# Kernel tuning notes

Measured on AMD Instinct MI355X. Metric: run time of the kernel, lower is better.

The kernel has to match this reference:

```python
import jax, jax.numpy as jnp
import numpy as np

D_CH = 2048  # channels
N = 64       # hidden_state
L = 8192     # sequence length
MIN_DELTA, MAX_DELTA = 1e-3, 0.1


def setup_inputs() -> dict:
    key = jax.random.key(0)
    ks = jax.random.split(key, 5)
    X = jax.random.normal(ks[0], (D_CH, L), jnp.float32)
    # kaiming_normal_(nonlinearity='linear'): std = 1/sqrt(fan_in=N)
    A = jax.random.normal(ks[1], (N, N), jnp.float32) * (1.0 / N) ** 0.5
    B = jax.random.normal(ks[2], (N, D_CH), jnp.float32) * (1.0 / N) ** 0.5
    C = jax.random.normal(ks[3], (D_CH, N), jnp.float32)
    Dp = jnp.ones((D_CH,), jnp.float32)
    log_delta = jax.random.uniform(ks[4], (1,), jnp.float32,
                                   float(np.log(MIN_DELTA)), float(np.log(MAX_DELTA)))
    return {"X": X, "A": A, "B": B, "C": C, "Dp": Dp, "log_delta": log_delta}


def reference(X, A, B, C, Dp, log_delta):
    # X: (D, L). Bilinear (Tustin) discretization with dt = exp(log_delta).
    n = A.shape[0]
    delta = jnp.exp(log_delta)[0]
    I = jnp.eye(n, dtype=A.dtype)
    inv = jnp.linalg.inv(I - (delta * 0.5) * A)
    dA = inv @ (I + (delta * 0.5) * A)      # (N, N)
    dB = delta * (inv @ B)                   # (N, D)

    def step(h, x_t):
        # h: (N,), x_t: (D,)
        h = dA @ h + dB @ x_t
        return h, C @ h                      # y_t: (D,)

    h0 = jnp.zeros((n,), X.dtype)
    _, ys = jax.lax.scan(step, h0, X.T)      # ys: (L, D)
    # skip connection y += D * X (per-channel)
    return ys.T + Dp[:, None] * X            # (D, L)
```

## Files before the change

kernel.cpp:

```cpp
#include <hip/hip_runtime.h>
#include <math.h>

#define D_CH 2048
#define LSEQ 8192
#define T1 32
#define NC1 256
#define VSLAB 524288

typedef __attribute__((ext_vector_type(8))) short bf16x8;
typedef __attribute__((ext_vector_type(4))) float f32x4;

__device__ __forceinline__ short f2bf(float x) {
  unsigned u = __float_as_uint(x);
  u += 0x7FFFu + ((u >> 16) & 1);
  return (short)(u >> 16);
}

__device__ __forceinline__ void mmzero(float acc[16]) {
#pragma unroll
  for (int t = 0; t < 16; ++t) acc[t] = 0.f;
}

template <int SZ>
__device__ __forceinline__ void mmld(float acc[16], const float* __restrict__ Z,
                                     int r0, int c0) {
#pragma unroll
  for (int i = 0; i < 4; ++i) {
    float4 z = *(const float4*)&Z[(r0 + i) * SZ + c0];
    acc[i * 4 + 0] = z.x; acc[i * 4 + 1] = z.y;
    acc[i * 4 + 2] = z.z; acc[i * 4 + 3] = z.w;
  }
}

template <int SX, int SY>
__device__ __forceinline__ void mac44(float acc[16], const float* __restrict__ Xb,
                                      const float* __restrict__ Yb, int r0, int c0) {
#pragma unroll 4
  for (int k = 0; k < 64; k += 4) {
    float4 x0 = *(const float4*)&Xb[(r0 + 0) * SX + k];
    float4 x1 = *(const float4*)&Xb[(r0 + 1) * SX + k];
    float4 x2 = *(const float4*)&Xb[(r0 + 2) * SX + k];
    float4 x3 = *(const float4*)&Xb[(r0 + 3) * SX + k];
    float4 y0 = *(const float4*)&Yb[(k + 0) * SY + c0];
    float4 y1 = *(const float4*)&Yb[(k + 1) * SY + c0];
    float4 y2 = *(const float4*)&Yb[(k + 2) * SY + c0];
    float4 y3 = *(const float4*)&Yb[(k + 3) * SY + c0];
#define MROW(i, xi) \
    acc[i * 4 + 0] += xi.x * y0.x + xi.y * y1.x + xi.z * y2.x + xi.w * y3.x; \
    acc[i * 4 + 1] += xi.x * y0.y + xi.y * y1.y + xi.z * y2.y + xi.w * y3.y; \
    acc[i * 4 + 2] += xi.x * y0.z + xi.y * y1.z + xi.z * y2.z + xi.w * y3.z; \
    acc[i * 4 + 3] += xi.x * y0.w + xi.y * y1.w + xi.z * y2.w + xi.w * y3.w;
    MROW(0, x0) MROW(1, x1) MROW(2, x2) MROW(3, x3)
#undef MROW
  }
}

template <int SZ>
__device__ __forceinline__ void mmst(float* Dst, const float acc[16], int r0, int c0) {
#pragma unroll
  for (int i = 0; i < 4; ++i)
    *(float4*)&Dst[(r0 + i) * SZ + c0] =
        make_float4(acc[i * 4 + 0], acc[i * 4 + 1], acc[i * 4 + 2], acc[i * 4 + 3]);
}

__global__ __launch_bounds__(256) void main_kernel(const float* __restrict__ X,
                                                   const float* __restrict__ A,
                                                   const float* __restrict__ B,
                                                   const float* __restrict__ logd,
                                                   float* __restrict__ invdT,
                                                   float* __restrict__ dAg,
                                                   float* __restrict__ V,
                                                   int KS) {
  __shared__ float smem[8704];
  const int tid = threadIdx.x;
  const int lane = tid & 63;
  const int w = tid >> 6;

  if (blockIdx.x == 0) {
    float* bQ = smem;
    float* bP = smem + 4352;
    const int r0 = (tid >> 4) * 4, c0 = (tid & 15) * 4;
    const float delta = expf(logd[0]);
    const float half = 0.5f * delta;
    float accQ[16], accP[16];

    for (int idx = tid; idx < 4096; idx += 256) {
      int i = idx >> 6, j = idx & 63;
      float p = half * A[idx];
      bP[i * 68 + j] = p;
      bQ[i * 68 + j] = p + (i == j ? 1.f : 0.f);
    }
    __syncthreads();
    mmzero(accP); mac44<68, 68>(accP, bP, bP, r0, c0);
    __syncthreads();
    mmst<68>(bP, accP, r0, c0);
    __syncthreads();
#pragma unroll 1
    for (int s = 0; s < 3; ++s) {
      mmld<68>(accQ, bQ, r0, c0);
      mac44<68, 68>(accQ, bP, bQ, r0, c0);
      if (s < 2) { mmzero(accP); mac44<68, 68>(accP, bP, bP, r0, c0); }
      __syncthreads();
      mmst<68>(bQ, accQ, r0, c0);
      if (s < 2) mmst<68>(bP, accP, r0, c0);
      __syncthreads();
    }

    for (int idx = tid; idx < 4096; idx += 256) {
      int n = idx >> 6, m = idx & 63;
      float qv = bQ[n * 68 + m];
      invdT[m * 64 + n] = delta * qv;
      dAg[idx] = 2.f * qv - (n == m ? 1.f : 0.f);
    }
    return;
  }

  const int b = blockIdx.x - 1;
  const int t0 = (b & 255) << 5;
  const int slab = b >> 8;
  const int k0 = slab * KS;
  short* Xs = (short*)smem;
  short* Bs = (short*)smem + 2304;
  const int q = lane >> 4, r = lane & 15;
  const int hi = lane >> 5, tl = lane & 31;
  const int brow = lane >> 3;
  const int bkc = (lane & 7) * 8;
  const int wm = (w & 1) * 16;
  const int wn = (w >> 1) * 32;

  f32x4 acc[2];
#pragma unroll
  for (int j = 0; j < 2; ++j) acc[j] = (f32x4){0.f, 0.f, 0.f, 0.f};

  float xv[8];
  float bv[16];

#define LOADX(KK)                                                              \
  _Pragma("unroll")                                                            \
  for (int j = 0; j < 8; ++j)                                                  \
    xv[j] = X[(size_t)(k0 + (KK) + w * 16 + hi * 8 + j) * LSEQ + t0 + tl];

#define LOADB(KK)                                                              \
  _Pragma("unroll")                                                            \
  for (int p = 0; p < 2; ++p) {                                                \
    int n = p * 32 + w * 8 + brow;                                             \
    float4 f0 = *(const float4*)&B[(size_t)n * D_CH + k0 + (KK) + bkc];        \
    float4 f1 = *(const float4*)&B[(size_t)n * D_CH + k0 + (KK) + bkc + 4];    \
    bv[p * 8 + 0] = f0.x; bv[p * 8 + 1] = f0.y;                                \
    bv[p * 8 + 2] = f0.z; bv[p * 8 + 3] = f0.w;                                \
    bv[p * 8 + 4] = f1.x; bv[p * 8 + 5] = f1.y;                                \
    bv[p * 8 + 6] = f1.z; bv[p * 8 + 7] = f1.w;                                \
  }

  LOADX(0)
  LOADB(0)

  for (int kk = 0; kk < KS; kk += 64) {
    bf16x8 xp;
#pragma unroll
    for (int j = 0; j < 8; ++j) xp[j] = f2bf(xv[j]);
    *(bf16x8*)&Xs[tl * 72 + w * 16 + hi * 8] = xp;
#pragma unroll
    for (int p = 0; p < 2; ++p) {
      bf16x8 bp8;
#pragma unroll
      for (int j = 0; j < 8; ++j) bp8[j] = f2bf(bv[p * 8 + j]);
      *(bf16x8*)&Bs[(p * 32 + w * 8 + brow) * 72 + bkc] = bp8;
    }
    __syncthreads();

    if (kk + 64 < KS) {
      LOADX(kk + 64)
      LOADB(kk + 64)
    }

#pragma unroll
    for (int ks = 0; ks < 64; ks += 32) {
      bf16x8 a = *(const bf16x8*)&Xs[(wm + r) * 72 + ks + q * 8];
#pragma unroll
      for (int j = 0; j < 2; ++j) {
        bf16x8 bb = *(const bf16x8*)&Bs[(wn + j * 16 + r) * 72 + ks + q * 8];
        acc[j] = __builtin_amdgcn_mfma_f32_16x16x32_bf16(a, bb, acc[j], 0, 0, 0);
      }
    }
    __syncthreads();
  }
#undef LOADX
#undef LOADB

  float* Vs = V + (size_t)slab * VSLAB;
#pragma unroll
  for (int j = 0; j < 2; ++j)
#pragma unroll
    for (int reg = 0; reg < 4; ++reg)
      Vs[(size_t)(t0 + wm + q * 4 + reg) * 64 + wn + j * 16 + r] = acc[j][reg];
}

__device__ __forceinline__ float matvec_lds(const float* __restrict__ Mrow,
                                            const float* __restrict__ hb, float u) {
  float a0 = u, a1 = 0.f, a2 = 0.f, a3 = 0.f;
#pragma unroll
  for (int jj = 0; jj < 64; jj += 4) {
    float4 m = *(const float4*)&Mrow[jj];
    float4 hv = *(const float4*)&hb[jj];
    a0 += m.x * hv.x;
    a1 += m.y * hv.y;
    a2 += m.z * hv.z;
    a3 += m.w * hv.w;
  }
  return (a0 + a1) + (a2 + a3);
}

__device__ __forceinline__ void stage_mat64(float* Mlds, const float* __restrict__ Mg,
                                            int lane) {
#pragma unroll
  for (int i = 0; i < 16; ++i) {
    int row = i * 4 + (lane >> 4);
    int col = (lane & 15) * 4;
    *(float4*)&Mlds[row * 68 + col] = *(const float4*)&Mg[row * 64 + col];
  }
  __syncthreads();
}

__global__ __launch_bounds__(256) void scan1_kernel(const float* __restrict__ V,
                                                    const float* __restrict__ invdT,
                                                    const float* __restrict__ dA,
                                                    float* __restrict__ U,
                                                    float* __restrict__ S,
                                                    float* __restrict__ dA32g,
                                                    float* __restrict__ dA512g,
                                                    int nslab) {
  __shared__ float smem[13056];
  const int tid = threadIdx.x;
  const int c = blockIdx.x;

  if (c == NC1) {
    float* b0 = smem;
    float* b1 = smem + 4352;
    const int r0 = (tid >> 4) * 4, c0 = (tid & 15) * 4;
    for (int idx = tid; idx < 4096; idx += 256)
      b0[(idx >> 6) * 68 + (idx & 63)] = dA[idx];
    __syncthreads();
    float acc[16];
    float* p = b0; float* q = b1;
    for (int s = 1; s <= 9; ++s) {
      mmzero(acc); mac44<68, 68>(acc, p, p, r0, c0);
      if (s == 5) mmst<64>(dA32g, acc, r0, c0);
      if (s == 9) mmst<64>(dA512g, acc, r0, c0);
      mmst<68>(q, acc, r0, c0);
      __syncthreads();
      float* t = p; p = q; q = t;
    }
    return;
  }

  float* invs = smem;
  float* Vs   = smem + 4096;
  float* Us   = smem + 6144;
  float* hs0  = smem + 8192;
  float* hs1  = smem + 8256;
  float* Md   = smem + 8320;

  for (int idx = tid; idx < 4096; idx += 256) invs[idx] = invdT[idx];
  for (int idx = tid; idx < 4096; idx += 256)
    Md[(idx >> 6) * 68 + (idx & 63)] = dA[idx];
  for (int idx = tid; idx < 2048; idx += 256) {
    float v = 0.f;
    for (int s = 0; s < nslab; ++s) v += V[(size_t)s * VSLAB + (size_t)c * 2048 + idx];
    Vs[idx] = v;
  }
  __syncthreads();

  const int r0 = (tid >> 4) * 2, c0 = (tid & 15) * 4;
  float a0[4] = {0.f, 0.f, 0.f, 0.f}, a1[4] = {0.f, 0.f, 0.f, 0.f};
#pragma unroll 4
  for (int k = 0; k < 64; k += 4) {
    float4 v0 = *(const float4*)&Vs[r0 * 64 + k];
    float4 v1 = *(const float4*)&Vs[(r0 + 1) * 64 + k];
    float4 y0 = *(const float4*)&invs[(k + 0) * 64 + c0];
    float4 y1 = *(const float4*)&invs[(k + 1) * 64 + c0];
    float4 y2 = *(const float4*)&invs[(k + 2) * 64 + c0];
    float4 y3 = *(const float4*)&invs[(k + 3) * 64 + c0];
    a0[0] += v0.x * y0.x + v0.y * y1.x + v0.z * y2.x + v0.w * y3.x;
    a0[1] += v0.x * y0.y + v0.y * y1.y + v0.z * y2.y + v0.w * y3.y;
    a0[2] += v0.x * y0.z + v0.y * y1.z + v0.z * y2.z + v0.w * y3.z;
    a0[3] += v0.x * y0.w + v0.y * y1.w + v0.z * y2.w + v0.w * y3.w;
    a1[0] += v1.x * y0.x + v1.y * y1.x + v1.z * y2.x + v1.w * y3.x;
    a1[1] += v1.x * y0.y + v1.y * y1.y + v1.z * y2.y + v1.w * y3.y;
    a1[2] += v1.x * y0.z + v1.y * y1.z + v1.z * y2.z + v1.w * y3.z;
    a1[3] += v1.x * y0.w + v1.y * y1.w + v1.z * y2.w + v1.w * y3.w;
  }
  *(float4*)&Us[r0 * 64 + c0] = make_float4(a0[0], a0[1], a0[2], a0[3]);
  *(float4*)&Us[(r0 + 1) * 64 + c0] = make_float4(a1[0], a1[1], a1[2], a1[3]);
  *(float4*)&U[(size_t)(c * 32 + r0) * 64 + c0] = make_float4(a0[0], a0[1], a0[2], a0[3]);
  *(float4*)&U[(size_t)(c * 32 + r0 + 1) * 64 + c0] = make_float4(a1[0], a1[1], a1[2], a1[3]);
  __syncthreads();

  if (tid < 64) {
    const float* row = Md + tid * 68;
    float h = 0.f;
    hs0[tid] = 0.f;
    for (int t = 0; t < T1; ++t) {
      float u = Us[t * 64 + tid];
      h = matvec_lds(row, (t & 1) ? hs1 : hs0, u);
      ((t & 1) ? hs0 : hs1)[tid] = h;
    }
    S[c * 64 + tid] = h;
  }
}

__global__ __launch_bounds__(64) void mid1_kernel(const float* __restrict__ S,
                                                  const float* __restrict__ dA32,
                                                  float* __restrict__ S2g) {
  __shared__ float M[64 * 68];
  __shared__ float hs[2][64];
  const int lane = threadIdx.x;
  const int g = blockIdx.x;
  stage_mat64(M, dA32, lane);
  const float* row = M + lane * 68;
  const float* in = S + g * 16 * 64;
  float h = 0.f;
  hs[0][lane] = 0.f;
  for (int t = 0; t < 16; ++t) {
    h = matvec_lds(row, hs[t & 1], in[t * 64 + lane]);
    hs[(t + 1) & 1][lane] = h;
  }
  S2g[g * 64 + lane] = h;
}

__global__ __launch_bounds__(64) void mid2_kernel(const float* __restrict__ S2g,
                                                  const float* __restrict__ dA512,
                                                  float* __restrict__ H2g) {
  __shared__ float M[64 * 68];
  __shared__ float hs[2][64];
  const int lane = threadIdx.x;
  stage_mat64(M, dA512, lane);
  const float* row = M + lane * 68;
  float h = 0.f;
  hs[0][lane] = 0.f;
  for (int t = 0; t < 16; ++t) {
    H2g[t * 64 + lane] = h;
    h = matvec_lds(row, hs[t & 1], S2g[t * 64 + lane]);
    hs[(t + 1) & 1][lane] = h;
  }
}

__global__ __launch_bounds__(64) void mid3_kernel(const float* __restrict__ S,
                                                  const float* __restrict__ dA32,
                                                  const float* __restrict__ H2g,
                                                  float* __restrict__ Hinit) {
  __shared__ float M[64 * 68];
  __shared__ float hs[2][64];
  const int lane = threadIdx.x;
  const int g = blockIdx.x;
  stage_mat64(M, dA32, lane);
  const float* row = M + lane * 68;
  const float* in = S + g * 16 * 64;
  float h = H2g[g * 64 + lane];
  hs[0][lane] = h;
  for (int t = 0; t < 16; ++t) {
    Hinit[(g * 16 + t) * 64 + lane] = h;
    h = matvec_lds(row, hs[t & 1], in[t * 64 + lane]);
    hs[(t + 1) & 1][lane] = h;
  }
}

__global__ __launch_bounds__(64) void scan2_kernel(const float* __restrict__ U,
                                                   const float* __restrict__ dA,
                                                   const float* __restrict__ Hinit,
                                                   float* __restrict__ Ht) {
  __shared__ float M[64 * 68];
  __shared__ float hs[2][64];
  const int tid = threadIdx.x;
  const int c = blockIdx.x;
  stage_mat64(M, dA, tid);
  const float* row = M + tid * 68;
  float h = Hinit[c * 64 + tid];
  hs[0][tid] = h;
  const float* inc = U + (size_t)c * T1 * 64;
  float* outc = Ht + (size_t)c * T1 * 64;
  float up[4];
#pragma unroll
  for (int i = 0; i < 4; ++i) up[i] = inc[i * 64 + tid];

  for (int t = 0; t < T1; ++t) {
    float u = up[t & 3];
    if (t + 4 < T1) up[t & 3] = inc[(t + 4) * 64 + tid];
    h = matvec_lds(row, hs[t & 1], u);
    hs[(t + 1) & 1][tid] = h;
    outc[t * 64 + tid] = h;
  }
}

__global__ __launch_bounds__(256) void out_kernel(const float* __restrict__ X,
                                                  const float* __restrict__ C,
                                                  const float* __restrict__ Dp,
                                                  const float* __restrict__ Ht,
                                                  float* __restrict__ Y) {
  __shared__ short Cs[64 * 72];
  __shared__ short Hs[64 * 72];
  const int tid = threadIdx.x;
  const int lane = tid & 63, w = tid >> 6;
  const int t0 = blockIdx.x * 64;
  const int d0 = blockIdx.y * 64;
  const int q = lane >> 4, r = lane & 15;
  const int brow = lane >> 3, bkc = (lane & 7) * 8;

#pragma unroll
  for (int p = 0; p < 2; ++p) {
    int row = p * 32 + w * 8 + brow;
    float4 c0 = *(const float4*)&C[(size_t)(d0 + row) * 64 + bkc];
    float4 c1 = *(const float4*)&C[(size_t)(d0 + row) * 64 + bkc + 4];
    float4 h0 = *(const float4*)&Ht[(size_t)(t0 + row) * 64 + bkc];
    float4 h1 = *(const float4*)&Ht[(size_t)(t0 + row) * 64 + bkc + 4];
    bf16x8 cv, hv;
    cv[0] = f2bf(c0.x); cv[1] = f2bf(c0.y); cv[2] = f2bf(c0.z); cv[3] = f2bf(c0.w);
    cv[4] = f2bf(c1.x); cv[5] = f2bf(c1.y); cv[6] = f2bf(c1.z); cv[7] = f2bf(c1.w);
    hv[0] = f2bf(h0.x); hv[1] = f2bf(h0.y); hv[2] = f2bf(h0.z); hv[3] = f2bf(h0.w);
    hv[4] = f2bf(h1.x); hv[5] = f2bf(h1.y); hv[6] = f2bf(h1.z); hv[7] = f2bf(h1.w);
    *(bf16x8*)&Cs[row * 72 + bkc] = cv;
    *(bf16x8*)&Hs[row * 72 + bkc] = hv;
  }
  __syncthreads();

  f32x4 acc[4];
#pragma unroll
  for (int j = 0; j < 4; ++j) acc[j] = (f32x4){0.f, 0.f, 0.f, 0.f};
#pragma unroll
  for (int ks = 0; ks < 64; ks += 32) {
    bf16x8 a = *(const bf16x8*)&Cs[(w * 16 + r) * 72 + ks + q * 8];
#pragma unroll
    for (int j = 0; j < 4; ++j) {
      bf16x8 bb = *(const bf16x8*)&Hs[(j * 16 + r) * 72 + ks + q * 8];
      acc[j] = __builtin_amdgcn_mfma_f32_16x16x32_bf16(a, bb, acc[j], 0, 0, 0);
    }
  }

#pragma unroll
  for (int reg = 0; reg < 4; ++reg) {
    int d = d0 + w * 16 + q * 4 + reg;
    float dp = Dp[d];
#pragma unroll
    for (int j = 0; j < 4; ++j) {
      int t = t0 + j * 16 + r;
      size_t off = (size_t)d * LSEQ + t;
      Y[off] = acc[j][reg] + dp * X[off];
    }
  }
}

extern "C" void kernel_launch(void* const* d_in, const int* in_sizes, int n_in,
                              void* d_out, int out_size, void* d_ws, size_t ws_size,
                              hipStream_t stream) {
  const float* X  = (const float*)d_in[0];
  const float* A  = (const float*)d_in[1];
  const float* B  = (const float*)d_in[2];
  const float* Cm = (const float*)d_in[3];
  const float* Dp = (const float*)d_in[4];
  const float* ld = (const float*)d_in[5];
  float* out = (float*)d_out;
  float* ws = (float*)d_ws;

  const size_t need4 =
      (size_t)(16384 + 4 * VSLAB + VSLAB + 16384 + 16384 + 2048) * 4;
  const int nslab = (ws_size >= need4) ? 4 : 2;

  float* invdT = ws;
  float* dA    = ws + 4096;
  float* dA32  = ws + 8192;
  float* dA512 = ws + 12288;
  float* V     = ws + 16384;
  float* U     = V + (size_t)nslab * VSLAB;
  float* S     = U + VSLAB;
  float* Hinit = S + 16384;
  float* S2g   = Hinit + 16384;
  float* H2g   = S2g + 1024;
  float* Ht    = V;

  main_kernel<<<nslab * 256 + 1, 256, 0, stream>>>(X, A, B, ld, invdT, dA, V,
                                                   2048 / nslab);
  scan1_kernel<<<NC1 + 1, 256, 0, stream>>>(V, invdT, dA, U, S, dA32, dA512, nslab);
  mid1_kernel<<<16, 64, 0, stream>>>(S, dA32, S2g);
  mid2_kernel<<<1, 64, 0, stream>>>(S2g, dA512, H2g);
  mid3_kernel<<<16, 64, 0, stream>>>(S, dA32, H2g, Hinit);
  scan2_kernel<<<NC1, 64, 0, stream>>>(U, dA, Hinit, Ht);
  out_kernel<<<dim3(128, 32), 256, 0, stream>>>(X, Cm, Dp, Ht, out);
}
```

Measured before the change: 223.1 us.

## Double-buffer LDS tiles in B*X GEMM and vectorize output epilogue via LDS

The input-projection GEMM now double-buffers its LDS tiles, so the next tile is converted and stored while MFMAs run on the current one. This removes one barrier per k-step. The LDS row pitch changes from 72 to 76 shorts in both GEMM kernels to alter the bank-conflict pattern. The output kernel now stages its accumulators through LDS and writes Y with coalesced float4 loads and stores, replacing the previous scalar strided accesses. These changes cost more LDS and extra barriers in the epilogue.

```diff
diff --git a/kernel.cpp b/kernel.cpp
--- a/kernel.cpp
+++ b/kernel.cpp
@@ -119,8 +119,7 @@
   const int t0 = (b & 255) << 5;
   const int slab = b >> 8;
   const int k0 = slab * KS;
-  short* Xs = (short*)smem;
-  short* Bs = (short*)smem + 2304;
+  short* XB = (short*)smem;
   const int q = lane >> 4, r = lane & 15;
   const int hi = lane >> 5, tl = lane & 31;
   const int brow = lane >> 3;
@@ -142,51 +141,62 @@
 
 #define LOADB(KK)                                                              \
   _Pragma("unroll")                                                            \
-  for (int p = 0; p < 2; ++p) {                                                \
-    int n = p * 32 + w * 8 + brow;                                             \
+  for (int pp = 0; pp < 2; ++pp) {                                             \
+    int n = pp * 32 + w * 8 + brow;                                            \
     float4 f0 = *(const float4*)&B[(size_t)n * D_CH + k0 + (KK) + bkc];        \
     float4 f1 = *(const float4*)&B[(size_t)n * D_CH + k0 + (KK) + bkc + 4];    \
-    bv[p * 8 + 0] = f0.x; bv[p * 8 + 1] = f0.y;                                \
-    bv[p * 8 + 2] = f0.z; bv[p * 8 + 3] = f0.w;                                \
-    bv[p * 8 + 4] = f1.x; bv[p * 8 + 5] = f1.y;                                \
-    bv[p * 8 + 6] = f1.z; bv[p * 8 + 7] = f1.w;                                \
+    bv[pp * 8 + 0] = f0.x; bv[pp * 8 + 1] = f0.y;                              \
+    bv[pp * 8 + 2] = f0.z; bv[pp * 8 + 3] = f0.w;                              \
+    bv[pp * 8 + 4] = f1.x; bv[pp * 8 + 5] = f1.y;                              \
+    bv[pp * 8 + 6] = f1.z; bv[pp * 8 + 7] = f1.w;                              \
+  }
+
+#define STORE_TILE(BUF)                                                        \
+  {                                                                            \
+    short* Xs_ = XB + (BUF) * 7296;                                            \
+    short* Bs_ = Xs_ + 2432;                                                   \
+    bf16x8 xp;                                                                 \
+    _Pragma("unroll")                                                          \
+    for (int j = 0; j < 8; ++j) xp[j] = f2bf(xv[j]);                           \
+    *(bf16x8*)&Xs_[tl * 76 + w * 16 + hi * 8] = xp;                            \
+    _Pragma("unroll")                                                          \
+    for (int pp = 0; pp < 2; ++pp) {                                           \
+      bf16x8 bp8;                                                              \
+      _Pragma("unroll")                                                        \
+      for (int j = 0; j < 8; ++j) bp8[j] = f2bf(bv[pp * 8 + j]);               \
+      *(bf16x8*)&Bs_[(pp * 32 + w * 8 + brow) * 76 + bkc] = bp8;               \
+    }                                                                          \
   }
 
   LOADX(0)
   LOADB(0)
+  STORE_TILE(0)
+  __syncthreads();
 
   for (int kk = 0; kk < KS; kk += 64) {
-    bf16x8 xp;
-#pragma unroll
-    for (int j = 0; j < 8; ++j) xp[j] = f2bf(xv[j]);
-    *(bf16x8*)&Xs[tl * 72 + w * 16 + hi * 8] = xp;
-#pragma unroll
-    for (int p = 0; p < 2; ++p) {
-      bf16x8 bp8;
-#pragma unroll
-      for (int j = 0; j < 8; ++j) bp8[j] = f2bf(bv[p * 8 + j]);
-      *(bf16x8*)&Bs[(p * 32 + w * 8 + brow) * 72 + bkc] = bp8;
-    }
-    __syncthreads();
-
-    if (kk + 64 < KS) {
+    const int cur = (kk >> 6) & 1;
+    const short* Xs = XB + cur * 7296;
+    const short* Bs = Xs + 2432;
+    const bool more = kk + 64 < KS;
+    if (more) {
       LOADX(kk + 64)
       LOADB(kk + 64)
     }
-
 #pragma unroll
     for (int ks = 0; ks < 64; ks += 32) {
-      bf16x8 a = *(const bf16x8*)&Xs[(wm + r) * 72 + ks + q * 8];
+      bf16x8 a = *(const bf16x8*)&Xs[(wm + r) * 76 + ks + q * 8];
 #pragma unroll
       for (int j = 0; j < 2; ++j) {
-        bf16x8 bb = *(const bf16x8*)&Bs[(wn + j * 16 + r) * 72 + ks + q * 8];
+        bf16x8 bb = *(const bf16x8*)&Bs[(wn + j * 16 + r) * 76 + ks + q * 8];
         acc[j] = __builtin_amdgcn_mfma_f32_16x16x32_bf16(a, bb, acc[j], 0, 0, 0);
       }
     }
+    if (more) STORE_TILE(cur ^ 1)
     __syncthreads();
   }
 #undef LOADX
 #undef LOADB
+#undef STORE_TILE
 
   float* Vs = V + (size_t)slab * VSLAB;
 #pragma unroll
@@ -397,8 +407,9 @@
                                                   const float* __restrict__ Dp,
                                                   const float* __restrict__ Ht,
                                                   float* __restrict__ Y) {
-  __shared__ short Cs[64 * 72];
-  __shared__ short Hs[64 * 72];
+  __shared__ float smem[4864];
+  short* Cs = (short*)smem;
+  short* Hs = (short*)smem + 4864;
   const int tid = threadIdx.x;
   const int lane = tid & 63, w = tid >> 6;
   const int t0 = blockIdx.x * 64;
@@ -418,8 +429,8 @@
     cv[4] = f2bf(c1.x); cv[5] = f2bf(c1.y); cv[6] = f2bf(c1.z); cv[7] = f2bf(c1.w);
     hv[0] = f2bf(h0.x); hv[1] = f2bf(h0.y); hv[2] = f2bf(h0.z); hv[3] = f2bf(h0.w);
     hv[4] = f2bf(h1.x); hv[5] = f2bf(h1.y); hv[6] = f2bf(h1.z); hv[7] = f2bf(h1.w);
-    *(bf16x8*)&Cs[row * 72 + bkc] = cv;
-    *(bf16x8*)&Hs[row * 72 + bkc] = hv;
+    *(bf16x8*)&Cs[row * 76 + bkc] = cv;
+    *(bf16x8*)&Hs[row * 76 + bkc] = hv;
   }
   __syncthreads();
 
@@ -428,24 +439,34 @@
   for (int j = 0; j < 4; ++j) acc[j] = (f32x4){0.f, 0.f, 0.f, 0.f};
 #pragma unroll
   for (int ks = 0; ks < 64; ks += 32) {
-    bf16x8 a = *(const bf16x8*)&Cs[(w * 16 + r) * 72 + ks + q * 8];
+    bf16x8 a = *(const bf16x8*)&Cs[(w * 16 + r) * 76 + ks + q * 8];
 #pragma unroll
     for (int j = 0; j < 4; ++j) {
-      bf16x8 bb = *(const bf16x8*)&Hs[(j * 16 + r) * 72 + ks + q * 8];
+      bf16x8 bb = *(const bf16x8*)&Hs[(j * 16 + r) * 76 + ks + q * 8];
       acc[j] = __builtin_amdgcn_mfma_f32_16x16x32_bf16(a, bb, acc[j], 0, 0, 0);
     }
   }
-
-#pragma unroll
-  for (int reg = 0; reg < 4; ++reg) {
-    int d = d0 + w * 16 + q * 4 + reg;
-    float dp = Dp[d];
-#pragma unroll
-    for (int j = 0; j < 4; ++j) {
-      int t = t0 + j * 16 + r;
-      size_t off = (size_t)d * LSEQ + t;
-      Y[off] = acc[j][reg] + dp * X[off];
-    }
+  __syncthreads();
+
+  float* Ts = smem;
+#pragma unroll
+  for (int reg = 0; reg < 4; ++reg)
+#pragma unroll
+    for (int j = 0; j < 4; ++j)
+      Ts[(w * 16 + q * 4 + reg) * 68 + j * 16 + r] = acc[j][reg];
+  __syncthreads();
+
+  const int rr = lane >> 4;
+  const int c4 = (lane & 15) * 4;
+#pragma unroll
+  for (int pass = 0; pass < 4; ++pass) {
+    int row = pass * 16 + w * 4 + rr;
+    float dp = Dp[d0 + row];
+    float4 v = *(const float4*)&Ts[row * 68 + c4];
+    size_t off = (size_t)(d0 + row) * LSEQ + t0 + c4;
+    float4 x = *(const float4*)&X[off];
+    *(float4*)&Y[off] = make_float4(v.x + dp * x.x, v.y + dp * x.y,
+                                    v.z + dp * x.z, v.w + dp * x.w);
   }
 }
 
```

Result: slower. 240.7 us (+7.9%).
